# Kernel optimization log

Hardware: AMD Instinct MI355X
Metric: run time of the kernel (lower is better)

The kernel has to match this reference:

```python
import jax, jax.numpy as jnp
import numpy as np

D_MODEL = 1024
SEQ = 4096

def setup_inputs() -> dict:
    key = jax.random.key(0)
    k_x, k_q, k_k, k_v, k_o = jax.random.split(key, 5)
    x = jax.random.normal(k_x, (SEQ, D_MODEL), dtype=jnp.float32)
    w_q = jax.random.normal(k_q, (D_MODEL, D_MODEL), dtype=jnp.float32)
    w_k = jax.random.normal(k_k, (D_MODEL, D_MODEL), dtype=jnp.float32)
    w_v = jax.random.normal(k_v, (D_MODEL, D_MODEL), dtype=jnp.float32)
    out_proj = jax.random.normal(k_o, (D_MODEL, D_MODEL), dtype=jnp.float32)
    return {"x": x, "w_q": w_q, "w_k": w_k, "w_v": w_v, "out_proj": out_proj}

def reference(x, w_q, w_k, w_v, out_proj):
    # Faithful to original: Q/K projections, scaled QK^T, softmax over last dim.
    # V and out_proj are computed/declared in the original module but unused in the output.
    Q = x @ w_q                      # [S, D]
    K = x @ w_k                      # [S, D]
    scale = 1.0 / jnp.sqrt(jnp.asarray(Q.shape[-1], dtype=Q.dtype))
    scores = (Q @ K.T) * scale       # [S, S]
    return jax.nn.softmax(scores, axis=-1)
```

## Files before the change

kernel.cpp:

```cpp
#include <hip/hip_runtime.h>
#include <math.h>

#define SEQ 4096
#define DM  1024

#define BM 128
#define BN 128
#define BK 16
#define PAD 4
#define NCT (SEQ / BN)
#define KS 32

typedef __attribute__((ext_vector_type(8))) short bf16x8;
typedef __attribute__((ext_vector_type(4))) float f32x4;

union U4 { uint4 u; unsigned short s[8]; };

__device__ __forceinline__ float bf2f(unsigned short u) {
    return __uint_as_float(((unsigned int)u) << 16);
}
__device__ __forceinline__ unsigned short f2bf(float f) {
    unsigned int u = __float_as_uint(f);
    return (unsigned short)((u + 0x7FFFu + ((u >> 16) & 1u)) >> 16);
}

__device__ __forceinline__ int detect_bf16(const void* p0) {
    const unsigned int* p = (const unsigned int*)p0;
    int cnt = 0;
    #pragma unroll
    for (int i = 0; i < 64; i++) {
        unsigned int e = (p[i] >> 7) & 0xFFu;
        cnt += (e >= 112u && e <= 140u) ? 1 : 0;
    }
    return cnt >= 48 ? 1 : 0;
}

__device__ __forceinline__ void load8(const void* base, size_t idx, int isbf, float* v) {
    if (isbf) {
        U4 t; t.u = *(const uint4*)((const unsigned short*)base + idx);
        #pragma unroll
        for (int q = 0; q < 8; q++) v[q] = bf2f(t.s[q]);
    } else {
        const float* f = (const float*)base + idx;
        float4 a = *(const float4*)f;
        float4 b = *(const float4*)(f + 4);
        v[0] = a.x; v[1] = a.y; v[2] = a.z; v[3] = a.w;
        v[4] = b.x; v[5] = b.y; v[6] = b.z; v[7] = b.w;
    }
}

__device__ __forceinline__ void gl16(const void* g, void* l) {
    __builtin_amdgcn_global_load_lds(
        (const __attribute__((address_space(1))) unsigned int*)g,
        (__attribute__((address_space(3))) unsigned int*)l, 16, 0, 0);
}

__global__ __launch_bounds__(256)
void xsplit_kernel(const void* __restrict__ X, unsigned short* __restrict__ Hi,
                   unsigned short* __restrict__ Lo)
{
    const int isbf = detect_bf16(X);
    size_t i = ((size_t)blockIdx.x * 256 + threadIdx.x) * 8;
    float v[8];
    load8(X, i, isbf, v);
    U4 h, l;
    #pragma unroll
    for (int q = 0; q < 8; q++) {
        h.s[q] = f2bf(v[q]);
        l.s[q] = f2bf(v[q] - bf2f(h.s[q]));
    }
    *(uint4*)(Hi + i) = h.u;
    *(uint4*)(Lo + i) = l.u;
}

__global__ __launch_bounds__(256)
void w2_part_kernel(const void* __restrict__ Wa, const void* __restrict__ Wb,
                    float* __restrict__ P, float scale)
{
    __shared__ float As[BK][BM + PAD];
    __shared__ float Bs[BK][BN + PAD];
    const int isa = detect_bf16(Wa);
    const int isb = detect_bf16(Wb);
    const int t  = threadIdx.x;
    const int bx = blockIdx.x;
    const int by = blockIdx.y;
    const int kz = blockIdx.z;
    const int tm = t >> 4, tn = t & 15;

    float acc[8][8];
    #pragma unroll
    for (int i = 0; i < 8; i++)
        #pragma unroll
        for (int j = 0; j < 8; j++) acc[i][j] = 0.f;

    const int ar = t >> 1;
    const int ak = (t & 1) * 8;
    const int k0 = kz * (DM / 4);

    for (int kt = k0; kt < k0 + DM / 4; kt += BK) {
        float av[8], bv[8];
        load8(Wa, (size_t)(by * BM + ar) * DM + kt + ak, isa, av);
        load8(Wb, (size_t)(bx * BN + ar) * DM + kt + ak, isb, bv);
        #pragma unroll
        for (int q = 0; q < 8; q++) As[ak + q][ar] = av[q];
        #pragma unroll
        for (int q = 0; q < 8; q++) Bs[ak + q][ar] = bv[q];
        __syncthreads();
        #pragma unroll
        for (int kk = 0; kk < BK; kk++) {
            float a[8], b[8];
            #pragma unroll
            for (int i = 0; i < 8; i++) a[i] = As[kk][tm * 8 + i];
            #pragma unroll
            for (int j = 0; j < 8; j++) b[j] = Bs[kk][tn * 8 + j];
            #pragma unroll
            for (int i = 0; i < 8; i++)
                #pragma unroll
                for (int j = 0; j < 8; j++)
                    acc[i][j] = fmaf(a[i], b[j], acc[i][j]);
        }
        __syncthreads();
    }
    float* base = P + (size_t)kz * DM * DM;
    #pragma unroll
    for (int i = 0; i < 8; i++) {
        float* cp = base + (size_t)(by * BM + tm * 8 + i) * DM + bx * BN + tn * 8;
        #pragma unroll
        for (int j = 0; j < 8; j++) cp[j] = acc[i][j] * scale;
    }
}

__global__ __launch_bounds__(256)
void w2_reduce_split_kernel(const float* __restrict__ P, unsigned short* __restrict__ Hi,
                            unsigned short* __restrict__ Lo)
{
    const size_t N = (size_t)DM * DM;
    size_t i = ((size_t)blockIdx.x * 256 + threadIdx.x) * 8;
    float v[8];
    #pragma unroll
    for (int h = 0; h < 8; h += 4) {
        float4 a = *(const float4*)(P + i + h);
        float4 b = *(const float4*)(P + N + i + h);
        float4 c = *(const float4*)(P + 2 * N + i + h);
        float4 d = *(const float4*)(P + 3 * N + i + h);
        v[h + 0] = a.x + b.x + c.x + d.x;
        v[h + 1] = a.y + b.y + c.y + d.y;
        v[h + 2] = a.z + b.z + c.z + d.z;
        v[h + 3] = a.w + b.w + c.w + d.w;
    }
    U4 h, l;
    #pragma unroll
    for (int q = 0; q < 8; q++) {
        h.s[q] = f2bf(v[q]);
        l.s[q] = f2bf(v[q] - bf2f(h.s[q]));
    }
    *(uint4*)(Hi + i) = h.u;
    *(uint4*)(Lo + i) = l.u;
}

__global__ __launch_bounds__(256)
void qw_mfma_kernel(const unsigned short* __restrict__ Ahi, const unsigned short* __restrict__ Alo,
                    const unsigned short* __restrict__ Bhi, const unsigned short* __restrict__ Blo,
                    float* __restrict__ O0, float* __restrict__ O1)
{
    __shared__ unsigned short lAhi[128 * KS];
    __shared__ unsigned short lAlo[128 * KS];
    __shared__ unsigned short lBhi[128 * KS];
    __shared__ unsigned short lBlo[128 * KS];

    const int t    = threadIdx.x;
    const int bx   = blockIdx.x;
    const int by   = blockIdx.y;
    const int kz   = blockIdx.z;
    const int lane = t & 63;
    const int w    = t >> 6;
    const int wr   = w >> 1;
    const int wc   = w & 1;
    const int fr   = lane & 15;
    const int fq   = lane >> 4;

    f32x4 acc[4][4];
    #pragma unroll
    for (int i = 0; i < 4; i++)
        #pragma unroll
        for (int j = 0; j < 4; j++)
            acc[i][j] = (f32x4){0.f, 0.f, 0.f, 0.f};

    const int trow = t >> 2;
    const int tcs  = t & 3;
    const int k0   = kz * (DM / 2);

    for (int kt = k0; kt < k0 + DM / 2; kt += KS) {
        #pragma unroll
        for (int p = 0; p < 2; p++) {
            const int row = p * 64 + trow;
            const int sc  = tcs ^ ((row >> 1) & 3);
            const int lof = (p * 256 + t) * 16;
            const size_t ga = (size_t)(by * BM + row) * DM + kt + sc * 8;
            const size_t gb = (size_t)(bx * BN + row) * DM + kt + sc * 8;
            gl16(Ahi + ga, (char*)lAhi + lof);
            gl16(Alo + ga, (char*)lAlo + lof);
            gl16(Bhi + gb, (char*)lBhi + lof);
            gl16(Blo + gb, (char*)lBlo + lof);
        }
        __syncthreads();

        bf16x8 bh[4], bl[4];
        #pragma unroll
        for (int nj = 0; nj < 4; nj++) {
            const int br = wc * 64 + nj * 16 + fr;
            const int bc = fq ^ ((br >> 1) & 3);
            bh[nj] = *(const bf16x8*)&lBhi[br * KS + bc * 8];
            bl[nj] = *(const bf16x8*)&lBlo[br * KS + bc * 8];
        }
        #pragma unroll
        for (int mi = 0; mi < 4; mi++) {
            const int ar_ = wr * 64 + mi * 16 + fr;
            const int ac_ = fq ^ ((ar_ >> 1) & 3);
            bf16x8 ah = *(const bf16x8*)&lAhi[ar_ * KS + ac_ * 8];
            bf16x8 al = *(const bf16x8*)&lAlo[ar_ * KS + ac_ * 8];
            #pragma unroll
            for (int nj = 0; nj < 4; nj++) {
                acc[mi][nj] = __builtin_amdgcn_mfma_f32_16x16x32_bf16(ah, bh[nj], acc[mi][nj], 0, 0, 0);
                acc[mi][nj] = __builtin_amdgcn_mfma_f32_16x16x32_bf16(al, bh[nj], acc[mi][nj], 0, 0, 0);
                acc[mi][nj] = __builtin_amdgcn_mfma_f32_16x16x32_bf16(ah, bl[nj], acc[mi][nj], 0, 0, 0);
                acc[mi][nj] = __builtin_amdgcn_mfma_f32_16x16x32_bf16(al, bl[nj], acc[mi][nj], 0, 0, 0);
            }
        }
        __syncthreads();
    }

    float* O = kz ? O1 : O0;
    #pragma unroll
    for (int mi = 0; mi < 4; mi++)
        #pragma unroll
        for (int reg = 0; reg < 4; reg++) {
            const int row = by * BM + wr * 64 + mi * 16 + fq * 4 + reg;
            #pragma unroll
            for (int nj = 0; nj < 4; nj++) {
                const int col = bx * BN + wc * 64 + nj * 16 + fr;
                O[(size_t)row * DM + col] = acc[mi][nj][reg];
            }
        }
}

__global__ __launch_bounds__(256)
void qw_combine_split_kernel(const float* __restrict__ P0, const float* __restrict__ P1,
                             unsigned short* __restrict__ Hi, unsigned short* __restrict__ Lo)
{
    size_t i = ((size_t)blockIdx.x * 256 + threadIdx.x) * 8;
    float4 a0 = *(const float4*)(P0 + i);
    float4 a1 = *(const float4*)(P0 + i + 4);
    float4 b0 = *(const float4*)(P1 + i);
    float4 b1 = *(const float4*)(P1 + i + 4);
    float v[8] = {a0.x + b0.x, a0.y + b0.y, a0.z + b0.z, a0.w + b0.w,
                  a1.x + b1.x, a1.y + b1.y, a1.z + b1.z, a1.w + b1.w};
    U4 h, l;
    #pragma unroll
    for (int q = 0; q < 8; q++) {
        h.s[q] = f2bf(v[q]);
        l.s[q] = f2bf(v[q] - bf2f(h.s[q]));
    }
    *(uint4*)(Hi + i) = h.u;
    *(uint4*)(Lo + i) = l.u;
}

__global__ __launch_bounds__(256)
void scores_mfma_kernel(const unsigned short* __restrict__ QWhi,
                        const unsigned short* __restrict__ QWlo,
                        const void* __restrict__ X,
                        float* __restrict__ pm, float* __restrict__ pl,
                        void* __restrict__ out)
{
    __shared__ unsigned short lAhi[128 * KS];
    __shared__ unsigned short lAlo[128 * KS];
    __shared__ unsigned short lBhi[128 * KS];
    __shared__ unsigned short lBlo[128 * KS];
    __shared__ float smax[128][2];
    __shared__ float ssum[128][2];

    const int isbf = detect_bf16(X);
    const int t    = threadIdx.x;
    const int bx   = blockIdx.x;
    const int by   = blockIdx.y;
    const int lane = t & 63;
    const int w    = t >> 6;
    const int wr   = w >> 1;
    const int wc   = w & 1;
    const int fr   = lane & 15;
    const int fq   = lane >> 4;

    f32x4 acc[4][4];
    #pragma unroll
    for (int i = 0; i < 4; i++)
        #pragma unroll
        for (int j = 0; j < 4; j++)
            acc[i][j] = (f32x4){0.f, 0.f, 0.f, 0.f};

    const int trow = t >> 2;
    const int tcs  = t & 3;

    for (int kt = 0; kt < DM; kt += KS) {
        #pragma unroll
        for (int p = 0; p < 2; p++) {
            const int row = p * 64 + trow;
            const int sc  = tcs ^ ((row >> 1) & 3);
            const int lof = (p * 256 + t) * 16;
            const size_t ga = (size_t)(by * BM + row) * DM + kt + sc * 8;
            gl16(QWhi + ga, (char*)lAhi + lof);
            gl16(QWlo + ga, (char*)lAlo + lof);
            if (isbf) {
                const size_t gb = (size_t)(bx * BN + row) * DM + kt + sc * 8;
                gl16((const unsigned short*)X + gb, (char*)lBhi + lof);
            }
        }
        if (!isbf) {
            const int row  = t >> 1;
            const int half = t & 1;
            const float* xp = (const float*)X + (size_t)(bx * BN + row) * DM + kt + half * 16;
            float4 v0 = ((const float4*)xp)[0];
            float4 v1 = ((const float4*)xp)[1];
            float4 v2 = ((const float4*)xp)[2];
            float4 v3 = ((const float4*)xp)[3];
            float vv[16] = {v0.x, v0.y, v0.z, v0.w, v1.x, v1.y, v1.z, v1.w,
                            v2.x, v2.y, v2.z, v2.w, v3.x, v3.y, v3.z, v3.w};
            U4 h0, h1, l0, l1;
            #pragma unroll
            for (int q = 0; q < 8; q++) {
                h0.s[q] = f2bf(vv[q]);
                l0.s[q] = f2bf(vv[q] - bf2f(h0.s[q]));
                h1.s[q] = f2bf(vv[8 + q]);
                l1.s[q] = f2bf(vv[8 + q] - bf2f(h1.s[q]));
            }
            const int s  = (row >> 1) & 3;
            const int ca = (2 * half) ^ s;
            const int cb = (2 * half + 1) ^ s;
            *(uint4*)&lBhi[row * KS + ca * 8] = h0.u;
            *(uint4*)&lBhi[row * KS + cb * 8] = h1.u;
            *(uint4*)&lBlo[row * KS + ca * 8] = l0.u;
            *(uint4*)&lBlo[row * KS + cb * 8] = l1.u;
        }
        __syncthreads();

        bf16x8 bh[4];
        #pragma unroll
        for (int nj = 0; nj < 4; nj++) {
            const int br = wc * 64 + nj * 16 + fr;
            const int bc = fq ^ ((br >> 1) & 3);
            bh[nj] = *(const bf16x8*)&lBhi[br * KS + bc * 8];
        }
        #pragma unroll
        for (int mi = 0; mi < 4; mi++) {
            const int ar_ = wr * 64 + mi * 16 + fr;
            const int ac_ = fq ^ ((ar_ >> 1) & 3);
            bf16x8 ah = *(const bf16x8*)&lAhi[ar_ * KS + ac_ * 8];
            bf16x8 al = *(const bf16x8*)&lAlo[ar_ * KS + ac_ * 8];
            #pragma unroll
            for (int nj = 0; nj < 4; nj++) {
                acc[mi][nj] = __builtin_amdgcn_mfma_f32_16x16x32_bf16(ah, bh[nj], acc[mi][nj], 0, 0, 0);
                acc[mi][nj] = __builtin_amdgcn_mfma_f32_16x16x32_bf16(al, bh[nj], acc[mi][nj], 0, 0, 0);
            }
        }
        if (!isbf) {
            bf16x8 bl[4];
            #pragma unroll
            for (int nj = 0; nj < 4; nj++) {
                const int br = wc * 64 + nj * 16 + fr;
                const int bc = fq ^ ((br >> 1) & 3);
                bl[nj] = *(const bf16x8*)&lBlo[br * KS + bc * 8];
            }
            #pragma unroll
            for (int mi = 0; mi < 4; mi++) {
                const int ar_ = wr * 64 + mi * 16 + fr;
                const int ac_ = fq ^ ((ar_ >> 1) & 3);
                bf16x8 ah = *(const bf16x8*)&lAhi[ar_ * KS + ac_ * 8];
                #pragma unroll
                for (int nj = 0; nj < 4; nj++)
                    acc[mi][nj] = __builtin_amdgcn_mfma_f32_16x16x32_bf16(ah, bl[nj], acc[mi][nj], 0, 0, 0);
            }
        }
        __syncthreads();
    }

    float rmx[4][4];
    #pragma unroll
    for (int mi = 0; mi < 4; mi++)
        #pragma unroll
        for (int reg = 0; reg < 4; reg++) {
            float m = acc[mi][0][reg];
            #pragma unroll
            for (int nj = 1; nj < 4; nj++) m = fmaxf(m, acc[mi][nj][reg]);
            m = fmaxf(m, __shfl_xor(m, 1, 64));
            m = fmaxf(m, __shfl_xor(m, 2, 64));
            m = fmaxf(m, __shfl_xor(m, 4, 64));
            m = fmaxf(m, __shfl_xor(m, 8, 64));
            rmx[mi][reg] = m;
        }
    if (fr == 0) {
        #pragma unroll
        for (int mi = 0; mi < 4; mi++)
            #pragma unroll
            for (int reg = 0; reg < 4; reg++)
                smax[wr * 64 + mi * 16 + fq * 4 + reg][wc] = rmx[mi][reg];
    }
    __syncthreads();
    float mt[4][4];
    #pragma unroll
    for (int mi = 0; mi < 4; mi++)
        #pragma unroll
        for (int reg = 0; reg < 4; reg++) {
            const int r = wr * 64 + mi * 16 + fq * 4 + reg;
            mt[mi][reg] = fmaxf(smax[r][0], smax[r][1]);
        }
    float rsm[4][4];
    #pragma unroll
    for (int mi = 0; mi < 4; mi++)
        #pragma unroll
        for (int reg = 0; reg < 4; reg++) rsm[mi][reg] = 0.f;
    #pragma unroll
    for (int mi = 0; mi < 4; mi++)
        #pragma unroll
        for (int nj = 0; nj < 4; nj++)
            #pragma unroll
            for (int reg = 0; reg < 4; reg++) {
                float e = __expf(acc[mi][nj][reg] - mt[mi][reg]);
                acc[mi][nj][reg] = e;
                rsm[mi][reg] += e;
            }
    #pragma unroll
    for (int mi = 0; mi < 4; mi++)
        #pragma unroll
        for (int reg = 0; reg < 4; reg++) {
            float s = rsm[mi][reg];
            s += __shfl_xor(s, 1, 64);
            s += __shfl_xor(s, 2, 64);
            s += __shfl_xor(s, 4, 64);
            s += __shfl_xor(s, 8, 64);
            if (fr == 0) ssum[wr * 64 + mi * 16 + fq * 4 + reg][wc] = s;
        }
    #pragma unroll
    for (int mi = 0; mi < 4; mi++)
        #pragma unroll
        for (int reg = 0; reg < 4; reg++) {
            const int row = by * BM + wr * 64 + mi * 16 + fq * 4 + reg;
            #pragma unroll
            for (int nj = 0; nj < 4; nj++) {
                const int col = bx * BN + wc * 64 + nj * 16 + fr;
                const float v = acc[mi][nj][reg];
                if (isbf)
                    ((unsigned short*)out)[(size_t)row * SEQ + col] = f2bf(v);
                else
                    ((float*)out)[(size_t)row * SEQ + col] = v;
            }
        }
    __syncthreads();
    if (t < 128) {
        const int grow = by * BM + t;
        pm[(size_t)bx * SEQ + grow] = fmaxf(smax[t][0], smax[t][1]);
        pl[(size_t)bx * SEQ + grow] = ssum[t][0] + ssum[t][1];
    }
}

__global__ __launch_bounds__(256)
void reduce_kernel(const float* __restrict__ pm, float* __restrict__ pl)
{
    int r = blockIdx.x * 256 + threadIdx.x;
    if (r >= SEQ) return;
    float m = pm[r];
    #pragma unroll
    for (int ti = 1; ti < NCT; ti++) m = fmaxf(m, pm[(size_t)ti * SEQ + r]);
    float l = 0.f;
    #pragma unroll
    for (int ti = 0; ti < NCT; ti++)
        l += pl[(size_t)ti * SEQ + r] * __expf(pm[(size_t)ti * SEQ + r] - m);
    float il = 1.f / l;
    #pragma unroll
    for (int ti = 0; ti < NCT; ti++)
        pl[(size_t)ti * SEQ + r] = __expf(pm[(size_t)ti * SEQ + r] - m) * il;
}

__global__ __launch_bounds__(256)
void fixup_kernel(const float* __restrict__ F, const void* __restrict__ X,
                  void* __restrict__ out)
{
    const int isbf = detect_bf16(X);
    size_t g = ((size_t)blockIdx.x * 256 + threadIdx.x) * 8;
    const int row = (int)(g >> 12);
    const int col = (int)(g & (SEQ - 1));
    const float f = F[(size_t)(col >> 7) * SEQ + row];
    if (isbf) {
        unsigned short* p = (unsigned short*)out + g;
        U4 v; v.u = *(const uint4*)p;
        #pragma unroll
        for (int q = 0; q < 8; q++) v.s[q] = f2bf(bf2f(v.s[q]) * f);
        *(uint4*)p = v.u;
    } else {
        float* p = (float*)out + g;
        float4 a = *(const float4*)p;
        float4 b = *(const float4*)(p + 4);
        a.x *= f; a.y *= f; a.z *= f; a.w *= f;
        b.x *= f; b.y *= f; b.z *= f; b.w *= f;
        *(float4*)p = a;
        *(float4*)(p + 4) = b;
    }
}

extern "C" void kernel_launch(void* const* d_in, const int* in_sizes, int n_in,
                              void* d_out, int out_size, void* d_ws, size_t ws_size,
                              hipStream_t stream)
{
    const void* x  = d_in[0];
    const void* wq = d_in[1];
    const void* wk = d_in[2];

    char* wsb = (char*)d_ws;
    char* dob = (char*)d_out;
    unsigned short* Xhi  = (unsigned short*)wsb;
    unsigned short* Xlo  = (unsigned short*)(wsb + ((size_t)8 << 20));
    float*          W2P  = (float*)(wsb + ((size_t)16 << 20));
    float*          QP0  = W2P;
    unsigned short* QWhi = (unsigned short*)wsb;
    unsigned short* QWlo = (unsigned short*)(wsb + ((size_t)8 << 20));
    float*          pm   = (float*)(wsb + ((size_t)16 << 20));
    float*          pl   = pm + (size_t)NCT * SEQ;
    unsigned short* W2Thi = (unsigned short*)dob;
    unsigned short* W2Tlo = (unsigned short*)(dob + ((size_t)2 << 20));
    float*          QP1   = (float*)(dob + ((size_t)16 << 20));

    dim3 blk(256);
    xsplit_kernel<<<dim3(SEQ * DM / (8 * 256)), blk, 0, stream>>>(x, Xhi, Xlo);
    w2_part_kernel<<<dim3(DM / BN, DM / BM, 4), blk, 0, stream>>>(wk, wq, W2P, 0.03125f);
    w2_reduce_split_kernel<<<dim3(DM * DM / (8 * 256)), blk, 0, stream>>>(W2P, W2Thi, W2Tlo);
    qw_mfma_kernel<<<dim3(DM / BN, SEQ / BM, 2), blk, 0, stream>>>(Xhi, Xlo, W2Thi, W2Tlo, QP0, QP1);
    qw_combine_split_kernel<<<dim3(SEQ * DM / (8 * 256)), blk, 0, stream>>>(QP0, QP1, QWhi, QWlo);
    scores_mfma_kernel<<<dim3(SEQ / BN, SEQ / BM), blk, 0, stream>>>(QWhi, QWlo, x, pm, pl, d_out);
    reduce_kernel<<<dim3(SEQ / 256), blk, 0, stream>>>(pm, pl);
    fixup_kernel<<<dim3(SEQ * SEQ / (8 * 256)), blk, 0, stream>>>(pl, x, d_out);
}
```

Baseline: 329.1 us.

## Compute W_k·W_qᵀ with split-bf16 MFMA and add workgroup swizzling

Replaces the scalar FP32 tiled GEMM that formed the Wk·Wqᵀ product with the split-bf16 MFMA kernel, generalized to take a k-chunk, partial stride and scale. A single split3 kernel converts x, Wq and Wk into hi/lo bf16 pairs in one launch. Workgroup IDs are remapped (swizzled) in the MFMA GEMMs and the scores kernel to improve L2 locality. Scratch buffers are reorganized across workspace and output memory, which costs some extra conversion traffic for the weights.

```diff
diff --git a/kernel.cpp b/kernel.cpp
--- a/kernel.cpp
+++ b/kernel.cpp
@@ -6,8 +6,6 @@
 
 #define BM 128
 #define BN 128
-#define BK 16
-#define PAD 4
 #define NCT (SEQ / BN)
 #define KS 32
 
@@ -56,13 +54,22 @@
 }
 
 __global__ __launch_bounds__(256)
-void xsplit_kernel(const void* __restrict__ X, unsigned short* __restrict__ Hi,
-                   unsigned short* __restrict__ Lo)
-{
-    const int isbf = detect_bf16(X);
-    size_t i = ((size_t)blockIdx.x * 256 + threadIdx.x) * 8;
+void split3_kernel(const void* __restrict__ X, const void* __restrict__ Wq,
+                   const void* __restrict__ Wk,
+                   unsigned short* __restrict__ Xhi, unsigned short* __restrict__ Xlo,
+                   unsigned short* __restrict__ Wqhi, unsigned short* __restrict__ Wqlo,
+                   unsigned short* __restrict__ Wkhi, unsigned short* __restrict__ Wklo)
+{
+    const int b = blockIdx.x;
+    const void* src;
+    unsigned short *Hi, *Lo;
+    size_t i;
+    if (b < 2048)      { src = X;  Hi = Xhi;  Lo = Xlo;  i = ((size_t)b * 256 + threadIdx.x) * 8; }
+    else if (b < 2560) { src = Wq; Hi = Wqhi; Lo = Wqlo; i = ((size_t)(b - 2048) * 256 + threadIdx.x) * 8; }
+    else               { src = Wk; Hi = Wkhi; Lo = Wklo; i = ((size_t)(b - 2560) * 256 + threadIdx.x) * 8; }
+    const int isbf = detect_bf16(src);
     float v[8];
-    load8(X, i, isbf, v);
+    load8(src, i, isbf, v);
     U4 h, l;
     #pragma unroll
     for (int q = 0; q < 8; q++) {
@@ -74,104 +81,25 @@
 }
 
 __global__ __launch_bounds__(256)
-void w2_part_kernel(const void* __restrict__ Wa, const void* __restrict__ Wb,
-                    float* __restrict__ P, float scale)
-{
-    __shared__ float As[BK][BM + PAD];
-    __shared__ float Bs[BK][BN + PAD];
-    const int isa = detect_bf16(Wa);
-    const int isb = detect_bf16(Wb);
-    const int t  = threadIdx.x;
-    const int bx = blockIdx.x;
-    const int by = blockIdx.y;
-    const int kz = blockIdx.z;
-    const int tm = t >> 4, tn = t & 15;
-
-    float acc[8][8];
-    #pragma unroll
-    for (int i = 0; i < 8; i++)
-        #pragma unroll
-        for (int j = 0; j < 8; j++) acc[i][j] = 0.f;
-
-    const int ar = t >> 1;
-    const int ak = (t & 1) * 8;
-    const int k0 = kz * (DM / 4);
-
-    for (int kt = k0; kt < k0 + DM / 4; kt += BK) {
-        float av[8], bv[8];
-        load8(Wa, (size_t)(by * BM + ar) * DM + kt + ak, isa, av);
-        load8(Wb, (size_t)(bx * BN + ar) * DM + kt + ak, isb, bv);
-        #pragma unroll
-        for (int q = 0; q < 8; q++) As[ak + q][ar] = av[q];
-        #pragma unroll
-        for (int q = 0; q < 8; q++) Bs[ak + q][ar] = bv[q];
-        __syncthreads();
-        #pragma unroll
-        for (int kk = 0; kk < BK; kk++) {
-            float a[8], b[8];
-            #pragma unroll
-            for (int i = 0; i < 8; i++) a[i] = As[kk][tm * 8 + i];
-            #pragma unroll
-            for (int j = 0; j < 8; j++) b[j] = Bs[kk][tn * 8 + j];
-            #pragma unroll
-            for (int i = 0; i < 8; i++)
-                #pragma unroll
-                for (int j = 0; j < 8; j++)
-                    acc[i][j] = fmaf(a[i], b[j], acc[i][j]);
-        }
-        __syncthreads();
-    }
-    float* base = P + (size_t)kz * DM * DM;
-    #pragma unroll
-    for (int i = 0; i < 8; i++) {
-        float* cp = base + (size_t)(by * BM + tm * 8 + i) * DM + bx * BN + tn * 8;
-        #pragma unroll
-        for (int j = 0; j < 8; j++) cp[j] = acc[i][j] * scale;
-    }
-}
-
-__global__ __launch_bounds__(256)
-void w2_reduce_split_kernel(const float* __restrict__ P, unsigned short* __restrict__ Hi,
-                            unsigned short* __restrict__ Lo)
-{
-    const size_t N = (size_t)DM * DM;
-    size_t i = ((size_t)blockIdx.x * 256 + threadIdx.x) * 8;
-    float v[8];
-    #pragma unroll
-    for (int h = 0; h < 8; h += 4) {
-        float4 a = *(const float4*)(P + i + h);
-        float4 b = *(const float4*)(P + N + i + h);
-        float4 c = *(const float4*)(P + 2 * N + i + h);
-        float4 d = *(const float4*)(P + 3 * N + i + h);
-        v[h + 0] = a.x + b.x + c.x + d.x;
-        v[h + 1] = a.y + b.y + c.y + d.y;
-        v[h + 2] = a.z + b.z + c.z + d.z;
-        v[h + 3] = a.w + b.w + c.w + d.w;
-    }
-    U4 h, l;
-    #pragma unroll
-    for (int q = 0; q < 8; q++) {
-        h.s[q] = f2bf(v[q]);
-        l.s[q] = f2bf(v[q] - bf2f(h.s[q]));
-    }
-    *(uint4*)(Hi + i) = h.u;
-    *(uint4*)(Lo + i) = l.u;
-}
-
-__global__ __launch_bounds__(256)
-void qw_mfma_kernel(const unsigned short* __restrict__ Ahi, const unsigned short* __restrict__ Alo,
-                    const unsigned short* __restrict__ Bhi, const unsigned short* __restrict__ Blo,
-                    float* __restrict__ O0, float* __restrict__ O1)
+void part_mfma_kernel(const unsigned short* __restrict__ Ahi, const unsigned short* __restrict__ Alo,
+                      const unsigned short* __restrict__ Bhi, const unsigned short* __restrict__ Blo,
+                      float* __restrict__ O, int kchunk, size_t pstride, float scale)
 {
     __shared__ unsigned short lAhi[128 * KS];
     __shared__ unsigned short lAlo[128 * KS];
     __shared__ unsigned short lBhi[128 * KS];
     __shared__ unsigned short lBlo[128 * KS];
 
-    const int t    = threadIdx.x;
-    const int bx   = blockIdx.x;
-    const int by   = blockIdx.y;
-    const int kz   = blockIdx.z;
+    const int t = threadIdx.x;
+    const int gy  = gridDim.y;
+    const int nwg = 8 * gy * gridDim.z;
+    const int lid = (blockIdx.z * gy + blockIdx.y) * 8 + blockIdx.x;
+    const int swz = (lid & 7) * (nwg >> 3) + (lid >> 3);
+    const int bx  = swz & 7;
+    const int rst = swz >> 3;
+    const int by  = rst % gy;
+    const int kz  = rst / gy;
+
     const int lane = t & 63;
     const int w    = t >> 6;
     const int wr   = w >> 1;
@@ -188,9 +116,9 @@
 
     const int trow = t >> 2;
     const int tcs  = t & 3;
-    const int k0   = kz * (DM / 2);
-
-    for (int kt = k0; kt < k0 + DM / 2; kt += KS) {
+    const int k0   = kz * kchunk;
+
+    for (int kt = k0; kt < k0 + kchunk; kt += KS) {
         #pragma unroll
         for (int p = 0; p < 2; p++) {
             const int row = p * 64 + trow;
@@ -230,7 +158,7 @@
         __syncthreads();
     }
 
-    float* O = kz ? O1 : O0;
+    float* Op = O + (size_t)kz * pstride;
     #pragma unroll
     for (int mi = 0; mi < 4; mi++)
         #pragma unroll
@@ -239,9 +167,37 @@
             #pragma unroll
             for (int nj = 0; nj < 4; nj++) {
                 const int col = bx * BN + wc * 64 + nj * 16 + fr;
-                O[(size_t)row * DM + col] = acc[mi][nj][reg];
-            }
-        }
+                Op[(size_t)row * DM + col] = acc[mi][nj][reg] * scale;
+            }
+        }
+}
+
+__global__ __launch_bounds__(256)
+void w2_reduce_split_kernel(const float* __restrict__ P, unsigned short* __restrict__ Hi,
+                            unsigned short* __restrict__ Lo)
+{
+    const size_t N = (size_t)DM * DM;
+    size_t i = ((size_t)blockIdx.x * 256 + threadIdx.x) * 8;
+    float v[8];
+    #pragma unroll
+    for (int h = 0; h < 8; h += 4) {
+        float4 a = *(const float4*)(P + i + h);
+        float4 b = *(const float4*)(P + N + i + h);
+        float4 c = *(const float4*)(P + 2 * N + i + h);
+        float4 d = *(const float4*)(P + 3 * N + i + h);
+        v[h + 0] = a.x + b.x + c.x + d.x;
+        v[h + 1] = a.y + b.y + c.y + d.y;
+        v[h + 2] = a.z + b.z + c.z + d.z;
+        v[h + 3] = a.w + b.w + c.w + d.w;
+    }
+    U4 h, l;
+    #pragma unroll
+    for (int q = 0; q < 8; q++) {
+        h.s[q] = f2bf(v[q]);
+        l.s[q] = f2bf(v[q] - bf2f(h.s[q]));
+    }
+    *(uint4*)(Hi + i) = h.u;
+    *(uint4*)(Lo + i) = l.u;
 }
 
 __global__ __launch_bounds__(256)
@@ -281,8 +237,10 @@
 
     const int isbf = detect_bf16(X);
     const int t    = threadIdx.x;
-    const int bx   = blockIdx.x;
-    const int by   = blockIdx.y;
+    const int lid  = blockIdx.y * 32 + blockIdx.x;
+    const int swz  = (lid & 7) * 128 + (lid >> 3);
+    const int bx   = swz & 31;
+    const int by   = swz >> 5;
     const int lane = t & 63;
     const int w    = t >> 6;
     const int wr   = w >> 1;
@@ -515,23 +473,30 @@
 
     char* wsb = (char*)d_ws;
     char* dob = (char*)d_out;
-    unsigned short* Xhi  = (unsigned short*)wsb;
-    unsigned short* Xlo  = (unsigned short*)(wsb + ((size_t)8 << 20));
-    float*          W2P  = (float*)(wsb + ((size_t)16 << 20));
-    float*          QP0  = W2P;
-    unsigned short* QWhi = (unsigned short*)wsb;
-    unsigned short* QWlo = (unsigned short*)(wsb + ((size_t)8 << 20));
-    float*          pm   = (float*)(wsb + ((size_t)16 << 20));
-    float*          pl   = pm + (size_t)NCT * SEQ;
-    unsigned short* W2Thi = (unsigned short*)dob;
-    unsigned short* W2Tlo = (unsigned short*)(dob + ((size_t)2 << 20));
-    float*          QP1   = (float*)(dob + ((size_t)16 << 20));
+    unsigned short* Xhi   = (unsigned short*)wsb;
+    unsigned short* Xlo   = (unsigned short*)(wsb + ((size_t)8 << 20));
+    unsigned short* QWhi  = (unsigned short*)wsb;
+    unsigned short* QWlo  = (unsigned short*)(wsb + ((size_t)8 << 20));
+    unsigned short* W2Thi = (unsigned short*)(wsb + ((size_t)16 << 20));
+    unsigned short* W2Tlo = (unsigned short*)(wsb + ((size_t)18 << 20));
+    float*          pm    = (float*)(wsb + ((size_t)16 << 20));
+    float*          pl    = pm + (size_t)NCT * SEQ;
+
+    unsigned short* Wkhi = (unsigned short*)dob;
+    unsigned short* Wklo = (unsigned short*)(dob + ((size_t)2 << 20));
+    unsigned short* Wqhi = (unsigned short*)(dob + ((size_t)4 << 20));
+    unsigned short* Wqlo = (unsigned short*)(dob + ((size_t)6 << 20));
+    float*          W2P  = (float*)(dob + ((size_t)8 << 20));
+    float*          QP0  = (float*)(dob + ((size_t)24 << 20));
+    float*          QP1  = QP0 + (size_t)SEQ * DM;
 
     dim3 blk(256);
-    xsplit_kernel<<<dim3(SEQ * DM / (8 * 256)), blk, 0, stream>>>(x, Xhi, Xlo);
-    w2_part_kernel<<<dim3(DM / BN, DM / BM, 4), blk, 0, stream>>>(wk, wq, W2P, 0.03125f);
+    split3_kernel<<<dim3(3072), blk, 0, stream>>>(x, wq, wk, Xhi, Xlo, Wqhi, Wqlo, Wkhi, Wklo);
+    part_mfma_kernel<<<dim3(8, DM / BM, 4), blk, 0, stream>>>(
+        Wkhi, Wklo, Wqhi, Wqlo, W2P, DM / 4, (size_t)DM * DM, 0.03125f);
     w2_reduce_split_kernel<<<dim3(DM * DM / (8 * 256)), blk, 0, stream>>>(W2P, W2Thi, W2Tlo);
-    qw_mfma_kernel<<<dim3(DM / BN, SEQ / BM, 2), blk, 0, stream>>>(Xhi, Xlo, W2Thi, W2Tlo, QP0, QP1);
+    part_mfma_kernel<<<dim3(8, SEQ / BM, 2), blk, 0, stream>>>(
+        Xhi, Xlo, W2Thi, W2Tlo, QP0, DM / 2, (size_t)SEQ * DM, 1.0f);
     qw_combine_split_kernel<<<dim3(SEQ * DM / (8 * 256)), blk, 0, stream>>>(QP0, QP1, QWhi, QWlo);
     scores_mfma_kernel<<<dim3(SEQ / BN, SEQ / BM), blk, 0, stream>>>(QWhi, QWlo, x, pm, pl, d_out);
     reduce_kernel<<<dim3(SEQ / 256), blk, 0, stream>>>(pm, pl);
```

Measured after the change: 305.9 us. -7.0%, faster.
